# Kernel tuning notes

Measured on AMD Instinct MI355X. Metric: run time of the kernel, lower is better.

Reference implementation:

```python
import jax, jax.numpy as jnp
import numpy as np

B, S, H = 2, 2048, 4096
NH, NKV, D = 32, 8, 128  # heads, kv heads, head_dim


def rotate_half(x):
    x1, x2 = jnp.split(x, 2, axis=-1)
    return jnp.concatenate((-x2, x1), axis=-1)


def setup_inputs() -> dict:
    key = jax.random.key(0)
    ks = jax.random.split(key, 5)
    hidden_states = jax.random.normal(ks[0], (B, S, H), jnp.float32) * 0.02
    wq = jax.random.normal(ks[1], (H, NH * D), jnp.float32) * 0.02
    wk = jax.random.normal(ks[2], (H, NKV * D), jnp.float32) * 0.02
    wv = jax.random.normal(ks[3], (H, NKV * D), jnp.float32) * 0.02
    wo = jax.random.normal(ks[4], (NH * D, H), jnp.float32) * 0.02
    # Llama rotary cache: emb = cat(freqs, freqs); cos/sin shape [S, D]
    inv_freq = 1.0 / (10000.0 ** (jnp.arange(0, D, 2, dtype=jnp.float32) / D))
    t = jnp.arange(S, dtype=jnp.float32)
    freqs = jnp.einsum('i,j->ij', t, inv_freq)
    emb = jnp.concatenate((freqs, freqs), axis=-1)
    cos, sin = jnp.cos(emb), jnp.sin(emb)
    # additive causal mask [S, S]
    causal = jnp.tril(jnp.ones((S, S), dtype=bool))
    attn_mask = jnp.where(causal, 0.0, -1e9).astype(jnp.float32)
    return {'hidden_states': hidden_states, 'wq': wq, 'wk': wk, 'wv': wv,
            'wo': wo, 'cos': cos, 'sin': sin, 'attn_mask': attn_mask}


def reference(hidden_states, wq, wk, wv, wo, cos, sin, attn_mask):
    b, s, _ = hidden_states.shape
    q = (hidden_states @ wq).reshape(b, s, NH, D)   # [b,s,nh,d]
    k = (hidden_states @ wk).reshape(b, s, NKV, D)  # [b,s,nkv,d]
    v = (hidden_states @ wv).reshape(b, s, NKV, D)
    c = cos[None, :, None, :]  # [1,s,1,d]
    sn = sin[None, :, None, :]
    q = q * c + rotate_half(q) * sn
    k = k * c + rotate_half(k) * sn
    # GQA: repeat KV heads to match query heads
    grp = NH // NKV
    k = jnp.repeat(k, grp, axis=2)
    v = jnp.repeat(v, grp, axis=2)
    scale = 1.0 / np.sqrt(D).astype(np.float32)
    scores = jnp.einsum('bqhd,bkhd->bhqk', q, k) * scale
    scores = scores + attn_mask[None, None, :, :]
    probs = jax.nn.softmax(scores, axis=-1)
    out = jnp.einsum('bhqk,bkhd->bqhd', probs, v).reshape(b, s, NH * D)
    return out @ wo
```

## Files before the change

kernel.cpp:

```cpp
#include <hip/hip_runtime.h>

typedef __attribute__((ext_vector_type(8))) short short8;
typedef __attribute__((ext_vector_type(4))) float f32x4;
typedef __attribute__((ext_vector_type(4))) int int4v;

__device__ __forceinline__ float bf2f(unsigned short u) {
  unsigned int x = ((unsigned int)u) << 16;
  float f;
  __builtin_memcpy(&f, &x, 4);
  return f;
}
__device__ __forceinline__ unsigned short f2bf(float f) {
  unsigned int x;
  __builtin_memcpy(&x, &f, 4);
  unsigned int r = (x + 0x7FFFu + ((x >> 16) & 1u)) >> 16;
  return (unsigned short)r;
}
__device__ __forceinline__ unsigned int cvtpk_bf16(float lo, float hi) {
  unsigned int r;
  asm("v_cvt_pk_bf16_f32 %0, %1, %2" : "=v"(r) : "v"(lo), "v"(hi));
  return r;
}
__device__ __forceinline__ float exp2_hw(float x) {
  float r;
  asm("v_exp_f32 %0, %1" : "=v"(r) : "v"(x));
  return r;
}
__device__ __forceinline__ int4v s8_to_i4(short8 v) {
  int4v r;
  __builtin_memcpy(&r, &v, 16);
  return r;
}
__device__ __forceinline__ short8 i4_to_s8(int4v v) {
  short8 r;
  __builtin_memcpy(&r, &v, 16);
  return r;
}
__device__ __forceinline__ short8 ld8_f32(const float* p) {
  f32x4 x = *(const f32x4*)p;
  f32x4 y = *(const f32x4*)(p + 4);
  short8 r;
  r[0] = (short)f2bf(x[0]); r[1] = (short)f2bf(x[1]);
  r[2] = (short)f2bf(x[2]); r[3] = (short)f2bf(x[3]);
  r[4] = (short)f2bf(y[0]); r[5] = (short)f2bf(y[1]);
  r[6] = (short)f2bf(y[2]); r[7] = (short)f2bf(y[3]);
  return r;
}

__device__ __forceinline__ void async16(unsigned short* lds, const unsigned short* g) {
  __builtin_amdgcn_global_load_lds(
      (const __attribute__((address_space(1))) void*)g,
      (__attribute__((address_space(3))) void*)lds, 16, 0, 0);
}

__global__ void downcast_f2b(const float* __restrict__ in,
                             unsigned short* __restrict__ out, int n8) {
  int i = blockIdx.x * 256 + threadIdx.x;
  if (i >= n8) return;
  *(short8*)(out + (size_t)i * 8) = ld8_f32(in + (size_t)i * 8);
}

__global__ void transpose64_f2b(const float* __restrict__ in,
                                unsigned short* __restrict__ out, int R, int C) {
  alignas(16) __shared__ unsigned short t[64][72];
  const int c0 = blockIdx.x * 64;
  const int r0 = blockIdx.y * 64;
  const int tid = threadIdx.x;
  const int rr = tid >> 4;
  const int cc = (tid & 15) << 2;
#pragma unroll
  for (int i = 0; i < 4; i++) {
    int r = rr + i * 16;
    f32x4 v = *(const f32x4*)(in + (size_t)(r0 + r) * C + c0 + cc);
#pragma unroll
    for (int j = 0; j < 4; j++) t[cc + j][r] = f2bf(v[j]);
  }
  __syncthreads();
  const int seg = tid & 7;
  const int cr = tid >> 3;
#pragma unroll
  for (int i = 0; i < 2; i++) {
    int c = cr + i * 32;
    short8 w = *(const short8*)&t[c][seg * 8];
    *(short8*)(out + (size_t)(c0 + c) * R + r0 + seg * 8) = w;
  }
}

#define MFMA16(AF, B0, B1, N0, N1)                                                   \
  _Pragma("unroll") for (int mi = 0; mi < 8; mi++) {                                 \
    acc[mi][N0] = __builtin_amdgcn_mfma_f32_16x16x32_bf16(AF[mi], B0, acc[mi][N0], 0, 0, 0); \
    acc[mi][N1] = __builtin_amdgcn_mfma_f32_16x16x32_bf16(AF[mi], B1, acc[mi][N1], 0, 0, 0); \
  }

#define STAGE8(BUF, SLOT, BASE, KOFF)                                     \
  do {                                                                    \
    async16(&lds[BUF][SLOT][tid * 8], (BASE) + (KOFF));                   \
    async16(&lds[BUF][SLOT][4096 + tid * 8], (BASE) + Kstep128 + (KOFF)); \
  } while (0)

#define BAR8 asm volatile("s_barrier" ::: "memory")

#define TILE8(CUR, UU, S0, S123, VM)                                                   \
  do {                                                                                 \
    const int kb = (UU)*64;                                                            \
    short8 af[8], b0, b1;                                                              \
                                                                       \
    _Pragma("unroll") for (int mi = 0; mi < 8; mi++)                                   \
        af[mi] = *(const short8*)(&lds[CUR][0][(wr * 128 + mi * 16 + fr) * 32 + fragoff]); \
    b0 = *(const short8*)(&lds[CUR][2][(wc * 64 + 0 * 16 + fr) * 32 + fragoff]);       \
    b1 = *(const short8*)(&lds[CUR][2][(wc * 64 + 1 * 16 + fr) * 32 + fragoff]);       \
    if (S0) STAGE8((CUR) ^ 1, 3, Bbase, kb + 96);                                      \
    BAR8;                                                                              \
    __builtin_amdgcn_s_setprio(1);                                                     \
    MFMA16(af, b0, b1, 0, 1);                                                          \
    __builtin_amdgcn_s_setprio(0);                                                     \
    BAR8;                                                                              \
                                                                       \
    b0 = *(const short8*)(&lds[CUR][2][(wc * 64 + 2 * 16 + fr) * 32 + fragoff]);       \
    b1 = *(const short8*)(&lds[CUR][2][(wc * 64 + 3 * 16 + fr) * 32 + fragoff]);       \
    if (S123) STAGE8(CUR, 0, Abase, kb + 128);                                         \
    BAR8;                                                                              \
    __builtin_amdgcn_s_setprio(1);                                                     \
    MFMA16(af, b0, b1, 2, 3);                                                          \
    __builtin_amdgcn_s_setprio(0);                                                     \
    BAR8;                                                                              \
                                                                       \
    _Pragma("unroll") for (int mi = 0; mi < 8; mi++)                                   \
        af[mi] = *(const short8*)(&lds[CUR][1][(wr * 128 + mi * 16 + fr) * 32 + fragoff]); \
    b0 = *(const short8*)(&lds[CUR][3][(wc * 64 + 0 * 16 + fr) * 32 + fragoff]);       \
    b1 = *(const short8*)(&lds[CUR][3][(wc * 64 + 1 * 16 + fr) * 32 + fragoff]);       \
    if (S123) STAGE8(CUR, 2, Bbase, kb + 128);                                         \
    BAR8;                                                                              \
    __builtin_amdgcn_s_setprio(1);                                                     \
    MFMA16(af, b0, b1, 0, 1);                                                          \
    __builtin_amdgcn_s_setprio(0);                                                     \
    BAR8;                                                                              \
                                                                       \
    b0 = *(const short8*)(&lds[CUR][3][(wc * 64 + 2 * 16 + fr) * 32 + fragoff]);       \
    b1 = *(const short8*)(&lds[CUR][3][(wc * 64 + 3 * 16 + fr) * 32 + fragoff]);       \
    if (S123) STAGE8(CUR, 1, Abase, kb + 160);                                         \
    BAR8;                                                                              \
    __builtin_amdgcn_s_setprio(1);                                                     \
    MFMA16(af, b0, b1, 2, 3);                                                          \
    __builtin_amdgcn_s_setprio(0);                                                     \
    if ((VM) == 6) {                                                                   \
      asm volatile("s_waitcnt vmcnt(6)" ::: "memory");                                 \
      __builtin_amdgcn_sched_barrier(0);                                               \
    } else if ((VM) == 0) {                                                            \
      asm volatile("s_waitcnt vmcnt(0)" ::: "memory");                                 \
      __builtin_amdgcn_sched_barrier(0);                                               \
    }                                                                                  \
    BAR8;                                                                              \
  } while (0)

template <int CF32>
__global__ __launch_bounds__(512, 2) void gemm8p(
    const unsigned short* __restrict__ A, const unsigned short* __restrict__ BT,
    void* __restrict__ Cp, int M, int N, int K) {
  alignas(16) __shared__ unsigned short lds[2][4][8192];
  const int tid = threadIdx.x;
  const int l = tid & 63;
  const int wv = tid >> 6;
  const int wr = wv >> 2, wc = wv & 3;

  const int nwg = gridDim.x * gridDim.y;
  int id = blockIdx.y * gridDim.x + blockIdx.x;
  id = (id & 7) * (nwg >> 3) + (id >> 3);
  const int bm = (id % gridDim.x) * 256;
  const int bn = (id / gridDim.x) * 256;

  const int fr = l & 15, hi = l >> 4;
  const int fragoff = ((hi ^ (((fr >> 3) & 1) << 1)) << 3);
  const int srow = tid >> 2;
  const int scol = (((tid & 3) ^ (((tid >> 5) & 1) << 1)) << 3);
  const unsigned short* Abase = A + (size_t)(bm + srow) * K + scol;
  const unsigned short* Bbase = BT + (size_t)(bn + srow) * K + scol;
  const size_t Kstep128 = (size_t)128 * K;

  f32x4 acc[8][4] = {};
  const int nt = K >> 6;

  STAGE8(0, 0, Abase, 0);
  STAGE8(0, 2, Bbase, 0);
  STAGE8(0, 1, Abase, 32);
  STAGE8(0, 3, Bbase, 32);
  STAGE8(1, 0, Abase, 64);
  STAGE8(1, 2, Bbase, 64);
  STAGE8(1, 1, Abase, 96);
  asm volatile("s_waitcnt vmcnt(6)" ::: "memory");
  __builtin_amdgcn_sched_barrier(0);
  BAR8;

  int U = 0;
  for (; U + 3 < nt; U += 2) {
    TILE8(0, U, 1, 1, 6);
    TILE8(1, U + 1, 1, 1, 6);
  }
  TILE8(0, nt - 2, 1, 0, 0);
  TILE8(1, nt - 1, 0, 0, -1);

  const int er = hi << 2;
#pragma unroll
  for (int mi = 0; mi < 8; mi++) {
#pragma unroll
    for (int ni = 0; ni < 4; ni++) {
      int row = bm + wr * 128 + mi * 16 + er;
      int col = bn + wc * 64 + ni * 16 + fr;
#pragma unroll
      for (int r = 0; r < 4; r++) {
        if constexpr (CF32)
          ((float*)Cp)[(size_t)(row + r) * N + col] = acc[mi][ni][r];
        else
          ((unsigned short*)Cp)[(size_t)(row + r) * N + col] = f2bf(acc[mi][ni][r]);
      }
    }
  }
}

__global__ void rope_qk(unsigned short* __restrict__ qkv,
                        const float* __restrict__ cosb,
                        const float* __restrict__ sinb, float qscale) {
  int gid = blockIdx.x * 256 + threadIdx.x;
  const int isK = gid >= 1048576;
  int g = isK ? gid - 1048576 : gid;
  const int nhs = isK ? 3 : 5;
  const int base = isK ? 4096 : 0;
  const float sc = isK ? 1.0f : qscale;
  int dblk = g & 7;
  int u2 = g >> 3;
  int head = u2 & ((1 << nhs) - 1);
  int token = u2 >> nhs;
  int s = token & 2047;
  int d0 = dblk << 3;
  unsigned short* p0 = qkv + (size_t)token * 6144 + base + (head << 7) + d0;
  unsigned short* p1 = p0 + 64;
  const float* cp = cosb + s * 128 + d0;
  const float* sp = sinb + s * 128 + d0;
  short8 a = *(const short8*)p0;
  short8 bq = *(const short8*)p1;
  f32x4 c0 = *(const f32x4*)cp, c1 = *(const f32x4*)(cp + 4);
  f32x4 s0 = *(const f32x4*)sp, s1 = *(const f32x4*)(sp + 4);
  short8 o0, o1;
#pragma unroll
  for (int j = 0; j < 8; j++) {
    float x0 = bf2f((unsigned short)a[j]);
    float x1 = bf2f((unsigned short)bq[j]);
    float c = (j < 4) ? c0[j & 3] : c1[j & 3];
    float sn = (j < 4) ? s0[j & 3] : s1[j & 3];
    o0[j] = (short)f2bf((x0 * c - x1 * sn) * sc);
    o1[j] = (short)f2bf((x1 * c + x0 * sn) * sc);
  }
  *(short8*)p0 = o0;
  *(short8*)p1 = o1;
}

#define NEGBIG -30000.0f

__device__ __forceinline__ int vswz(int d) { return (((d >> 3) ^ d) & 7) << 2; }

__global__ __launch_bounds__(256, 2) void flash_attn(
    const unsigned short* __restrict__ QKV, unsigned short* __restrict__ O) {
  alignas(16) __shared__ unsigned short lK[64 * 128];
  alignas(16) __shared__ unsigned int lV[128 * 32];

  const int tid = threadIdx.x;
  const int lane = tid & 63;
  const int w = tid >> 6;
  const int b = blockIdx.z;
  const int h = blockIdx.y;
  const int xa = blockIdx.x;
  const int kvh = h >> 2;

  const int fr = lane & 15;
  const int hi = lane >> 4;
  const int fk8 = hi << 3;
  const int hi4 = hi << 2;

  const int srow = tid >> 4;
  const int sc8 = (tid & 15) << 3;
  const int parity = srow & 1;

  const unsigned short* Kbp = QKV + (size_t)(b * 2048) * 6144 + 4096 + kvh * 128;
  const unsigned short* Vbp = Kbp + 1024;

  for (int pass = 0; pass < 2; pass++) {
    const int x = pass ? (15 - xa) : xa;
    const int q0 = x * 128;
    const int nt = 2 * x + 2;

    short8 qf[2][4];
#pragma unroll
    for (int qsub = 0; qsub < 2; qsub++) {
      const unsigned short* qb =
          QKV + (size_t)(b * 2048 + q0 + w * 32 + qsub * 16 + fr) * 6144 + h * 128 + fk8;
#pragma unroll
      for (int ks = 0; ks < 4; ks++) qf[qsub][ks] = *(const short8*)(qb + ks * 32);
    }

    f32x4 oacc[2][8] = {};
    float m2[2] = {NEGBIG, NEGBIG};
    float ls[2] = {0.f, 0.f};

    short8 kreg[4], vreg[4];
#pragma unroll
    for (int rep = 0; rep < 4; rep++) {
      kreg[rep] = *(const short8*)(Kbp + (size_t)(rep * 16 + srow) * 6144 + sc8);
      vreg[rep] = *(const short8*)(Vbp + (size_t)(rep * 16 + srow) * 6144 + sc8);
    }

    for (int t = 0; t < nt; t++) {
      __syncthreads();
#pragma unroll
      for (int rep = 0; rep < 4; rep++)
        *(short8*)(lK + (rep * 16 + srow) * 128 + (sc8 ^ ((srow & 7) << 3))) = kreg[rep];
#pragma unroll
      for (int rep = 0; rep < 4; rep++) {
        int4v own = s8_to_i4(vreg[rep]);
        int4v oth;
#pragma unroll
        for (int q = 0; q < 4; q++) oth[q] = __shfl_xor(own[q], 16);
        unsigned int oA = parity ? (unsigned)own[2] : (unsigned)own[0];
        unsigned int oB = parity ? (unsigned)own[3] : (unsigned)own[1];
        unsigned int tA = parity ? (unsigned)oth[2] : (unsigned)oth[0];
        unsigned int tB = parity ? (unsigned)oth[3] : (unsigned)oth[1];
        unsigned int evA = parity ? tA : oA, odA = parity ? oA : tA;
        unsigned int evB = parity ? tB : oB, odB = parity ? oB : tB;
        int d0 = sc8 + (parity << 2);
        int kvp = rep * 8 + (srow >> 1);
        lV[(d0 + 0) * 32 + (kvp ^ vswz(d0 + 0))] = (evA & 0xFFFFu) | (odA << 16);
        lV[(d0 + 1) * 32 + (kvp ^ vswz(d0 + 1))] = (evA >> 16) | (odA & 0xFFFF0000u);
        lV[(d0 + 2) * 32 + (kvp ^ vswz(d0 + 2))] = (evB & 0xFFFFu) | (odB << 16);
        lV[(d0 + 3) * 32 + (kvp ^ vswz(d0 + 3))] = (evB >> 16) | (odB & 0xFFFF0000u);
      }
      __syncthreads();

      if (t + 1 < nt) {
        const int kv1 = (t + 1) * 64;
#pragma unroll
        for (int rep = 0; rep < 4; rep++) {
          kreg[rep] = *(const short8*)(Kbp + (size_t)(kv1 + rep * 16 + srow) * 6144 + sc8);
          vreg[rep] = *(const short8*)(Vbp + (size_t)(kv1 + rep * 16 + srow) * 6144 + sc8);
        }
      } else if (pass == 0) {
#pragma unroll
        for (int rep = 0; rep < 4; rep++) {
          kreg[rep] = *(const short8*)(Kbp + (size_t)(rep * 16 + srow) * 6144 + sc8);
          vreg[rep] = *(const short8*)(Vbp + (size_t)(rep * 16 + srow) * 6144 + sc8);
        }
      }

      f32x4 sacc[2][4] = {};
      __builtin_amdgcn_s_setprio(1);
#pragma unroll
      for (int fc = 0; fc < 4; fc++)
#pragma unroll
        for (int ks = 0; ks < 4; ks++) {
          short8 bk = *(const short8*)(lK + (fc * 16 + fr) * 128 +
                                       ((ks * 32 + fk8) ^ ((fr & 7) << 3)));
          sacc[0][fc] = __builtin_amdgcn_mfma_f32_16x16x32_bf16(bk, qf[0][ks], sacc[0][fc], 0, 0, 0);
          sacc[1][fc] = __builtin_amdgcn_mfma_f32_16x16x32_bf16(bk, qf[1][ks], sacc[1][fc], 0, 0, 0);
        }
      __builtin_amdgcn_s_setprio(0);

      const bool diag = (t >= nt - 2);
      const int kvb = t * 64;
      unsigned int pk[2][4][2];

#pragma unroll
      for (int qsub = 0; qsub < 2; qsub++) {
        const int q = q0 + w * 32 + qsub * 16 + fr;
        float sv[4][4];
#pragma unroll
        for (int fc = 0; fc < 4; fc++)
#pragma unroll
          for (int r = 0; r < 4; r++) {
            float xx = sacc[qsub][fc][r];
            if (diag && (kvb + fc * 16 + hi4 + r > q)) xx = NEGBIG;
            sv[fc][r] = xx;
          }
        float mx = sv[0][0];
#pragma unroll
        for (int fc = 0; fc < 4; fc++)
#pragma unroll
          for (int r = 0; r < 4; r++) mx = fmaxf(mx, sv[fc][r]);
        mx = fmaxf(mx, __shfl_xor(mx, 16));
        mx = fmaxf(mx, __shfl_xor(mx, 32));
        if (__any(mx > m2[qsub] + 8.0f)) {
          float mnew = fmaxf(m2[qsub], mx);
          float alpha = exp2_hw(m2[qsub] - mnew);
          m2[qsub] = mnew;
          ls[qsub] *= alpha;
          f32x4 av;
#pragma unroll
          for (int r = 0; r < 4; r++) av[r] = __shfl(alpha, hi4 + r);
#pragma unroll
          for (int nf = 0; nf < 8; nf++) oacc[qsub][nf] *= av;
        }
        float rs = 0.f;
        float p[4][4];
#pragma unroll
        for (int fc = 0; fc < 4; fc++)
#pragma unroll
          for (int r = 0; r < 4; r++) {
            p[fc][r] = exp2_hw(sv[fc][r] - m2[qsub]);
            rs += p[fc][r];
          }
        rs += __shfl_xor(rs, 16);
        rs += __shfl_xor(rs, 32);
        ls[qsub] += rs;
#pragma unroll
        for (int fc = 0; fc < 4; fc++) {
          pk[qsub][fc][0] = cvtpk_bf16(p[fc][0], p[fc][1]);
          pk[qsub][fc][1] = cvtpk_bf16(p[fc][2], p[fc][3]);
        }
      }

      const int src0 = fr + ((hi & 1) << 5);
      const int src1 = src0 + 16;
#pragma unroll
      for (int kvs = 0; kvs < 2; kvs++) {
        unsigned int aw[2][4];
#pragma unroll
        for (int qsub = 0; qsub < 2; qsub++) {
#pragma unroll
          for (int jj = 0; jj < 4; jj++) {
            int src = (jj < 2) ? src0 : src1;
            int rr = jj & 1;
            unsigned int y0 = (unsigned)__shfl((int)pk[qsub][kvs * 2][rr], src);
            unsigned int y1 = (unsigned)__shfl((int)pk[qsub][kvs * 2 + 1][rr], src);
            aw[qsub][jj] = (hi >> 1) ? y1 : y0;
          }
        }
        int4v a0i = {(int)aw[0][0], (int)aw[0][1], (int)aw[0][2], (int)aw[0][3]};
        int4v a1i = {(int)aw[1][0], (int)aw[1][1], (int)aw[1][2], (int)aw[1][3]};
        short8 af0 = i4_to_s8(a0i), af1 = i4_to_s8(a1i);
        __builtin_amdgcn_s_setprio(1);
#pragma unroll
        for (int nf = 0; nf < 8; nf++) {
          int row = nf * 16 + fr;
          int4v bvw = *(const int4v*)(lV + row * 32 + ((kvs * 16 + hi4) ^ vswz(row)));
          short8 bv = i4_to_s8(bvw);
          oacc[0][nf] = __builtin_amdgcn_mfma_f32_16x16x32_bf16(af0, bv, oacc[0][nf], 0, 0, 0);
          oacc[1][nf] = __builtin_amdgcn_mfma_f32_16x16x32_bf16(af1, bv, oacc[1][nf], 0, 0, 0);
        }
        __builtin_amdgcn_s_setprio(0);
      }
    }

#pragma unroll
    for (int qsub = 0; qsub < 2; qsub++) {
      f32x4 iv;
#pragma unroll
      for (int r = 0; r < 4; r++) iv[r] = 1.0f / __shfl(ls[qsub], hi4 + r);
#pragma unroll
      for (int r = 0; r < 4; r++) {
        unsigned short* op =
            O + (size_t)(b * 2048 + q0 + w * 32 + qsub * 16 + hi4 + r) * 4096 + h * 128 + fr;
#pragma unroll
        for (int nf = 0; nf < 8; nf++) op[nf * 16] = f2bf(oacc[qsub][nf][r] * iv[r]);
      }
    }
  }
}

extern "C" void kernel_launch(void* const* d_in, const int* in_sizes, int n_in,
                              void* d_out, int out_size, void* d_ws, size_t ws_size,
                              hipStream_t stream) {
  const float* hs = (const float*)d_in[0];
  const float* wq = (const float*)d_in[1];
  const float* wk = (const float*)d_in[2];
  const float* wv = (const float*)d_in[3];
  const float* wo = (const float*)d_in[4];
  const float* cosb = (const float*)d_in[5];
  const float* sinb = (const float*)d_in[6];

  unsigned short* ws = (unsigned short*)d_ws;
  unsigned short* T1 = ws;
  unsigned short* T2 = T1 + 16777216;
  unsigned short* T3 = T2 + 4194304;
  unsigned short* QKV = T3 + 4194304;
  unsigned short* Ob = QKV + 25165824;

  unsigned short* hsb = (unsigned short*)d_out;

  downcast_f2b<<<8192, 256, 0, stream>>>(hs, hsb, 2097152);
  transpose64_f2b<<<dim3(64, 64), 256, 0, stream>>>(wq, T1, 4096, 4096);
  transpose64_f2b<<<dim3(16, 64), 256, 0, stream>>>(wk, T2, 4096, 1024);
  transpose64_f2b<<<dim3(16, 64), 256, 0, stream>>>(wv, T3, 4096, 1024);

  gemm8p<0><<<dim3(16, 24), 512, 0, stream>>>(hsb, T1, QKV, 4096, 6144, 4096);

  transpose64_f2b<<<dim3(64, 64), 256, 0, stream>>>(wo, T1, 4096, 4096);

  const float qscale = 0.08838834764831845f * 1.4426950408889634f;
  rope_qk<<<5120, 256, 0, stream>>>(QKV, cosb, sinb, qscale);

  flash_attn<<<dim3(8, 32, 2), 256, 0, stream>>>(QKV, Ob);

  gemm8p<1><<<dim3(16, 16), 512, 0, stream>>>(Ob, T1, (float*)d_out, 4096, 4096, 4096);
}
```

Baseline: 529.3 us.

## Double-buffer K/V shared memory and prepack V ahead of next tile

Shared-memory K and V tiles are now double-buffered, indexed by tile parity, which removes the leading barrier in each KV iteration so one barrier per tile remains. The V shuffle/packing work is moved out of the store phase and done after the PV MFMAs on the prefetched registers, so the LDS write at the next iteration is a plain store. The initial K/V prefetch is hoisted before the pass loop. This doubles LDS use (K+V ~32KB per block), which may pressure occupancy at two blocks per CU, and it relies on the single barrier being enough to avoid write-after-read hazards on the alternate buffer.

```diff
diff --git a/kernel.cpp b/kernel.cpp
--- a/kernel.cpp
+++ b/kernel.cpp
@@ -258,10 +258,31 @@
 
 __device__ __forceinline__ int vswz(int d) { return (((d >> 3) ^ d) & 7) << 2; }
 
+__device__ __forceinline__ void packV(const short8 vreg[4], int parity,
+                                      unsigned int vw[4][4]) {
+#pragma unroll
+  for (int rep = 0; rep < 4; rep++) {
+    int4v own = s8_to_i4(vreg[rep]);
+    int4v oth;
+#pragma unroll
+    for (int q = 0; q < 4; q++) oth[q] = __shfl_xor(own[q], 16);
+    unsigned int oA = parity ? (unsigned)own[2] : (unsigned)own[0];
+    unsigned int oB = parity ? (unsigned)own[3] : (unsigned)own[1];
+    unsigned int tA = parity ? (unsigned)oth[2] : (unsigned)oth[0];
+    unsigned int tB = parity ? (unsigned)oth[3] : (unsigned)oth[1];
+    unsigned int evA = parity ? tA : oA, odA = parity ? oA : tA;
+    unsigned int evB = parity ? tB : oB, odB = parity ? oB : tB;
+    vw[rep][0] = (evA & 0xFFFFu) | (odA << 16);
+    vw[rep][1] = (evA >> 16) | (odA & 0xFFFF0000u);
+    vw[rep][2] = (evB & 0xFFFFu) | (odB << 16);
+    vw[rep][3] = (evB >> 16) | (odB & 0xFFFF0000u);
+  }
+}
+
 __global__ __launch_bounds__(256, 2) void flash_attn(
     const unsigned short* __restrict__ QKV, unsigned short* __restrict__ O) {
-  alignas(16) __shared__ unsigned short lK[64 * 128];
-  alignas(16) __shared__ unsigned int lV[128 * 32];
+  alignas(16) __shared__ unsigned short lK[2][64 * 128];
+  alignas(16) __shared__ unsigned int lV[2][128 * 32];
 
   const int tid = threadIdx.x;
   const int lane = tid & 63;
@@ -279,9 +300,20 @@
   const int srow = tid >> 4;
   const int sc8 = (tid & 15) << 3;
   const int parity = srow & 1;
+  const int vd0 = sc8 + (parity << 2);
 
   const unsigned short* Kbp = QKV + (size_t)(b * 2048) * 6144 + 4096 + kvh * 128;
   const unsigned short* Vbp = Kbp + 1024;
+
+  short8 kreg[4], vreg[4];
+  unsigned int vw[4][4];
+
+#pragma unroll
+  for (int rep = 0; rep < 4; rep++) {
+    kreg[rep] = *(const short8*)(Kbp + (size_t)(rep * 16 + srow) * 6144 + sc8);
+    vreg[rep] = *(const short8*)(Vbp + (size_t)(rep * 16 + srow) * 6144 + sc8);
+  }
+  packV(vreg, parity, vw);
 
   for (int pass = 0; pass < 2; pass++) {
     const int x = pass ? (15 - xa) : xa;
@@ -301,36 +333,17 @@
     float m2[2] = {NEGBIG, NEGBIG};
     float ls[2] = {0.f, 0.f};
 
-    short8 kreg[4], vreg[4];
-#pragma unroll
-    for (int rep = 0; rep < 4; rep++) {
-      kreg[rep] = *(const short8*)(Kbp + (size_t)(rep * 16 + srow) * 6144 + sc8);
-      vreg[rep] = *(const short8*)(Vbp + (size_t)(rep * 16 + srow) * 6144 + sc8);
-    }
-
     for (int t = 0; t < nt; t++) {
-      __syncthreads();
+      const int c = t & 1;
 #pragma unroll
       for (int rep = 0; rep < 4; rep++)
-        *(short8*)(lK + (rep * 16 + srow) * 128 + (sc8 ^ ((srow & 7) << 3))) = kreg[rep];
+        *(short8*)(&lK[c][(rep * 16 + srow) * 128 + (sc8 ^ ((srow & 7) << 3))]) = kreg[rep];
 #pragma unroll
       for (int rep = 0; rep < 4; rep++) {
-        int4v own = s8_to_i4(vreg[rep]);
-        int4v oth;
-#pragma unroll
-        for (int q = 0; q < 4; q++) oth[q] = __shfl_xor(own[q], 16);
-        unsigned int oA = parity ? (unsigned)own[2] : (unsigned)own[0];
-        unsigned int oB = parity ? (unsigned)own[3] : (unsigned)own[1];
-        unsigned int tA = parity ? (unsigned)oth[2] : (unsigned)oth[0];
-        unsigned int tB = parity ? (unsigned)oth[3] : (unsigned)oth[1];
-        unsigned int evA = parity ? tA : oA, odA = parity ? oA : tA;
-        unsigned int evB = parity ? tB : oB, odB = parity ? oB : tB;
-        int d0 = sc8 + (parity << 2);
         int kvp = rep * 8 + (srow >> 1);
-        lV[(d0 + 0) * 32 + (kvp ^ vswz(d0 + 0))] = (evA & 0xFFFFu) | (odA << 16);
-        lV[(d0 + 1) * 32 + (kvp ^ vswz(d0 + 1))] = (evA >> 16) | (odA & 0xFFFF0000u);
-        lV[(d0 + 2) * 32 + (kvp ^ vswz(d0 + 2))] = (evB & 0xFFFFu) | (odB << 16);
-        lV[(d0 + 3) * 32 + (kvp ^ vswz(d0 + 3))] = (evB >> 16) | (odB & 0xFFFF0000u);
+#pragma unroll
+        for (int j = 0; j < 4; j++)
+          lV[c][(vd0 + j) * 32 + (kvp ^ vswz(vd0 + j))] = vw[rep][j];
       }
       __syncthreads();
 
@@ -355,8 +368,8 @@
       for (int fc = 0; fc < 4; fc++)
 #pragma unroll
         for (int ks = 0; ks < 4; ks++) {
-          short8 bk = *(const short8*)(lK + (fc * 16 + fr) * 128 +
-                                       ((ks * 32 + fk8) ^ ((fr & 7) << 3)));
+          short8 bk = *(const short8*)(&lK[c][(fc * 16 + fr) * 128 +
+                                              ((ks * 32 + fk8) ^ ((fr & 7) << 3))]);
           sacc[0][fc] = __builtin_amdgcn_mfma_f32_16x16x32_bf16(bk, qf[0][ks], sacc[0][fc], 0, 0, 0);
           sacc[1][fc] = __builtin_amdgcn_mfma_f32_16x16x32_bf16(bk, qf[1][ks], sacc[1][fc], 0, 0, 0);
         }
@@ -438,13 +451,15 @@
 #pragma unroll
         for (int nf = 0; nf < 8; nf++) {
           int row = nf * 16 + fr;
-          int4v bvw = *(const int4v*)(lV + row * 32 + ((kvs * 16 + hi4) ^ vswz(row)));
+          int4v bvw = *(const int4v*)(&lV[c][row * 32 + ((kvs * 16 + hi4) ^ vswz(row))]);
           short8 bv = i4_to_s8(bvw);
           oacc[0][nf] = __builtin_amdgcn_mfma_f32_16x16x32_bf16(af0, bv, oacc[0][nf], 0, 0, 0);
           oacc[1][nf] = __builtin_amdgcn_mfma_f32_16x16x32_bf16(af1, bv, oacc[1][nf], 0, 0, 0);
         }
         __builtin_amdgcn_s_setprio(0);
       }
+
+      packV(vreg, parity, vw);
     }
 
 #pragma unroll
```

After: 530.8 us. No clear change (+0.3%).
